# Optimization experiments

Measured on AMD Instinct MI355X. Metric: run time of the kernel, lower is better.

Reference implementation:

```python
import jax, jax.numpy as jnp
import numpy as np

B, P, K, HE, HF = 256, 128, 512, 1024, 512
D = K + HE + 2 * HF  # 2560, MLP input dim
HID = 64


def setup_inputs() -> dict:
    key = jax.random.key(0)
    ks = jax.random.split(key, 6)
    query = jax.random.normal(ks[0], (B, 1, HE), dtype=jnp.float32)
    keys = jax.random.normal(ks[1], (B, P, K), dtype=jnp.float32)
    frameLSTM_h = jax.random.normal(ks[2], (B, 1, 2 * HF), dtype=jnp.float32)
    mask = jax.random.randint(ks[3], (B, P), 0, 2, dtype=jnp.int32)
    mask = mask.at[:, 0].set(1)  # guarantee at least one unmasked player per row
    W1 = jax.random.normal(ks[4], (D, HID), dtype=jnp.float32) / np.float32(np.sqrt(D))
    W2 = jax.random.normal(ks[5], (HID, 1), dtype=jnp.float32) / np.float32(np.sqrt(HID))
    return dict(query=query, keys=keys, frameLSTM_h=frameLSTM_h, mask=mask, W1=W1, W2=W2)


def reference(query, keys, frameLSTM_h, mask, W1, W2):
    # Faithful to: cat([keys, query.repeat, frame.repeat]) @ W1 -> ReLU -> @ W2.
    # The pre-activation is linear, so splitting W1 by row-blocks is exactly the
    # same math without materializing the repeated/concatenated (B,P,D) tensor.
    W1k = W1[:K]            # (K, 64)
    W1q = W1[K:K + HE]      # (HE, 64)
    W1f = W1[K + HE:]       # (2*HF, 64)
    h = jax.nn.relu(
        jnp.einsum('bpk,kh->bph', keys, W1k)
        + jnp.einsum('boe,eh->boh', query, W1q)        # broadcasts over P
        + jnp.einsum('bof,fh->boh', frameLSTM_h, W1f)  # broadcasts over P
    )  # (B, P, 64)
    raw_scores = jnp.einsum('bph,ho->bp', h, W2)  # (B, P)
    raw_scores = jnp.where(mask == 0, -jnp.inf, raw_scores)
    weights = jax.nn.softmax(raw_scores, axis=1)  # (B, P)
    context = jnp.einsum('bp,bpk->bk', weights, keys)[:, None, :]  # (B, 1, K)
    embeddings = jnp.concatenate([context, frameLSTM_h], axis=2)   # (B, 1, K+2*HF)
    return embeddings, weights
```

## Files before the change

kernel.cpp:

```cpp
#include <hip/hip_runtime.h>
#include <hip/hip_bf16.h>
#include <cstdint>
#include <math.h>


typedef __bf16 bf16;
typedef __attribute__((ext_vector_type(8))) __bf16 bf16x8;
typedef __attribute__((ext_vector_type(4))) __bf16 bf16x4;
typedef __attribute__((ext_vector_type(4))) float f32x4;

#define NB 256
#define NP 128
#define NK 512
#define SKLD 520
#define SK_BYTES (NP * SKLD * 2)
#define SMEM_BYTES (SK_BYTES + 128*4 + 128*4 + 64*4 + 64*4)

__global__ __launch_bounds__(256) void prep_kernel(
    const float* __restrict__ query, const float* __restrict__ frame,
    const float* __restrict__ W1, bf16* __restrict__ w1kt,
    float* __restrict__ proj_part)
{
    const int blk = blockIdx.x;
    const int t = threadIdx.x;
    if (blk < 1024) {
        __shared__ float part[4][64];
        const int b = blk >> 2;
        const int q4 = blk & 3;
        const int h = t & 63;
        const int g = t >> 6;
        const float* src = (q4 < 2 ? query : frame) + (size_t)b * 1024 + (q4 & 1) * 512 + g * 128;
        const float* wrow = W1 + (size_t)(512 + q4 * 512 + g * 128) * 64 + h;
        float acc = 0.f;
#pragma unroll 8
        for (int dd = 0; dd < 128; dd++)
            acc += src[dd] * wrow[(size_t)dd * 64];
        part[g][h] = acc;
        __syncthreads();
        if (t < 64)
            proj_part[((size_t)q4 * NB + b) * 64 + t] =
                part[0][t] + part[1][t] + part[2][t] + part[3][t];
    } else {
        __shared__ float s[32][65];
        const int j = blk - 1024;
        const int k0 = j * 32;
#pragma unroll
        for (int i = 0; i < 8; i++) {
            const int idx = t + 256 * i;
            const int k = idx >> 6, h = idx & 63;
            s[k][h] = W1[(size_t)(k0 + k) * 64 + h];
        }
        __syncthreads();
#pragma unroll
        for (int i = 0; i < 8; i++) {
            const int idx = t + 256 * i;
            const int h = idx >> 5, kk = idx & 31;
            w1kt[(size_t)h * 512 + k0 + kk] = (bf16)s[kk][h];
        }
    }
}

__global__ __launch_bounds__(256) void attn_kernel(
    const float* __restrict__ keys, const float* __restrict__ frame,
    const int* __restrict__ mask, const float* __restrict__ W2,
    const bf16* __restrict__ w1kt, const float* __restrict__ proj_part,
    float* __restrict__ out)
{
    extern __shared__ char smem[];
    bf16* sk      = (bf16*)smem;
    float* scores = (float*)(smem + SK_BYTES);
    float* wts    = scores + 128;
    float* projl  = wts + 128;
    float* w2l    = projl + 64;

    const int b = blockIdx.x;
    const int t = threadIdx.x;

    if (t < 64)
        projl[t] = proj_part[(size_t)b * 64 + t]
                 + proj_part[((size_t)NB + b) * 64 + t]
                 + proj_part[((size_t)2 * NB + b) * 64 + t]
                 + proj_part[((size_t)3 * NB + b) * 64 + t];
    else if (t < 128) w2l[t - 64] = W2[t - 64];

    const float* kb = keys + (size_t)b * (NP * NK);
    {
        const int rowadd = t >> 7;
        const int c0 = (t & 127) * 4;
        float4 kv[2][16];
#pragma unroll
        for (int ii = 0; ii < 16; ii++)
            kv[0][ii] = *(const float4*)(kb + (size_t)ii * 1024 + t * 4);
#pragma unroll
        for (int jj = 0; jj < 4; jj++) {
            const int cur = jj & 1;
            if (jj < 3) {
#pragma unroll
                for (int ii = 0; ii < 16; ii++)
                    kv[cur ^ 1][ii] =
                        *(const float4*)(kb + (size_t)((jj + 1) * 16 + ii) * 1024 + t * 4);
            }
#pragma unroll
            for (int ii = 0; ii < 16; ii++) {
                const float4 v = kv[cur][ii];
                bf16x4 bv;
                bv[0] = (bf16)v.x; bv[1] = (bf16)v.y;
                bv[2] = (bf16)v.z; bv[3] = (bf16)v.w;
                *(bf16x4*)(sk + (size_t)(2 * (jj * 16 + ii) + rowadd) * SKLD + c0) = bv;
            }
        }
    }
    __syncthreads();

    const int w = t >> 6;
    const int lane = t & 63;
    const int m = lane & 15;
    const int q = lane >> 4;
    const int pw = w * 32;

    const bf16* bbase = w1kt + (size_t)m * 512 + q * 8;

    bf16x8 Bv[2][16];
#pragma unroll
    for (int kk = 0; kk < 16; kk++)
        Bv[0][kk] = *(const bf16x8*)(bbase + kk * 32);

    float pr[2][4] = {{0.f,0.f,0.f,0.f},{0.f,0.f,0.f,0.f}};

#pragma unroll
    for (int nt = 0; nt < 4; nt++) {
        const int cur = nt & 1;
        if (nt < 3) {
#pragma unroll
            for (int kk = 0; kk < 16; kk++)
                Bv[cur ^ 1][kk] = *(const bf16x8*)(bbase + (nt + 1) * 8192 + kk * 32);
        }
        f32x4 acc0 = (f32x4){0.f,0.f,0.f,0.f};
        f32x4 acc1 = (f32x4){0.f,0.f,0.f,0.f};
#pragma unroll
        for (int kk = 0; kk < 16; kk++) {
            const int k0 = kk * 32 + q * 8;
            const bf16x8 A0 = *(const bf16x8*)(sk + (pw + m) * SKLD + k0);
            const bf16x8 A1 = *(const bf16x8*)(sk + (pw + 16 + m) * SKLD + k0);
            acc0 = __builtin_amdgcn_mfma_f32_16x16x32_bf16(A0, Bv[cur][kk], acc0, 0, 0, 0);
            acc1 = __builtin_amdgcn_mfma_f32_16x16x32_bf16(A1, Bv[cur][kk], acc1, 0, 0, 0);
        }
        const int h = nt * 16 + m;
        const float pv = projl[h];
        const float wv = w2l[h];
#pragma unroll
        for (int r = 0; r < 4; r++) {
            pr[0][r] += fmaxf(acc0[r] + pv, 0.f) * wv;
            pr[1][r] += fmaxf(acc1[r] + pv, 0.f) * wv;
        }
    }

#pragma unroll
    for (int off = 1; off < 16; off <<= 1) {
#pragma unroll
        for (int mt = 0; mt < 2; mt++)
#pragma unroll
            for (int r = 0; r < 4; r++)
                pr[mt][r] += __shfl_xor(pr[mt][r], off);
    }
    if (m == 0) {
#pragma unroll
        for (int mt = 0; mt < 2; mt++) {
            const int pbase = pw + mt * 16 + q * 4;
#pragma unroll
            for (int r = 0; r < 4; r++) scores[pbase + r] = pr[mt][r];
        }
    }
    __syncthreads();

    if (w == 0) {
        const int pa = lane, pb = lane + 64;
        float s0 = (mask[b * 128 + pa] == 0) ? -INFINITY : scores[pa];
        float s1 = (mask[b * 128 + pb] == 0) ? -INFINITY : scores[pb];
        float mx = fmaxf(s0, s1);
#pragma unroll
        for (int off = 32; off; off >>= 1) mx = fmaxf(mx, __shfl_xor(mx, off));
        float e0 = __expf(s0 - mx), e1 = __expf(s1 - mx);
        float sum = e0 + e1;
#pragma unroll
        for (int off = 32; off; off >>= 1) sum += __shfl_xor(sum, off);
        const float inv = 1.0f / sum;
        e0 *= inv; e1 *= inv;
        wts[pa] = e0; wts[pb] = e1;
        float* wout = out + (size_t)NB * 1536;
        wout[b * 128 + pa] = e0;
        wout[b * 128 + pb] = e1;
    }
    __syncthreads();

    {
        float a0 = 0.f, a1 = 0.f;
        const int c = 2 * t;
#pragma unroll 8
        for (int p = 0; p < 128; p++) {
            const float wv = wts[p];
            const uint32_t uv = *(const uint32_t*)(sk + p * SKLD + c);
            a0 += wv * __uint_as_float(uv << 16);
            a1 += wv * __uint_as_float(uv & 0xffff0000u);
        }
        out[(size_t)b * 1536 + c] = a0;
        out[(size_t)b * 1536 + c + 1] = a1;
    }
    {
        const float4 fv = *(const float4*)(frame + (size_t)b * 1024 + t * 4);
        *(float4*)(out + (size_t)b * 1536 + 512 + t * 4) = fv;
    }
}

extern "C" void kernel_launch(void* const* d_in, const int* in_sizes, int n_in,
                              void* d_out, int out_size, void* d_ws, size_t ws_size,
                              hipStream_t stream) {
    const float* query = (const float*)d_in[0];
    const float* keys  = (const float*)d_in[1];
    const float* frame = (const float*)d_in[2];
    const int*   mask  = (const int*)d_in[3];
    const float* W1    = (const float*)d_in[4];
    const float* W2    = (const float*)d_in[5];
    float* out = (float*)d_out;

    bf16*  w1kt      = (bf16*)d_ws;
    float* proj_part = (float*)((char*)d_ws + (64 << 10));

    hipFuncSetAttribute((const void*)attn_kernel,
                        hipFuncAttributeMaxDynamicSharedMemorySize, SMEM_BYTES);

    prep_kernel<<<1040, 256, 0, stream>>>(query, frame, W1, w1kt, proj_part);
    attn_kernel<<<256, 256, SMEM_BYTES, stream>>>(keys, frame, mask, W2, w1kt,
                                                  proj_part, out);
}
```

Before: 123.5 us.

## Fold query/frame projection into attention kernel via MFMA on transposed bf16 W1

Moves the per-batch query/frame projection out of the 1024-block prep kernel and into the attention kernel. Each wave computes one 512-wide slice with bf16 MFMA, using only the broadcast row of the 16x16 tile. The prep kernel now only transposes W1 into bf16 layouts for the key and query/frame parts. This drops most of the prep grid and the proj_part round trip through global memory. In exchange, the projection now runs in bf16 instead of fp32, and the attention kernel does redundant MFMA work because 15 of the 16 rows are unused.

Result: no change. 123.1 us (-0.3%).

```diff
diff --git a/kernel.cpp b/kernel.cpp
--- a/kernel.cpp
+++ b/kernel.cpp
@@ -14,36 +14,17 @@
 #define NK 512
 #define SKLD 520
 #define SK_BYTES (NP * SKLD * 2)
-#define SMEM_BYTES (SK_BYTES + 128*4 + 128*4 + 64*4 + 64*4)
+#define SMEM_BYTES (SK_BYTES + 128*4 + 128*4 + 256*4 + 64*4)
 
 __global__ __launch_bounds__(256) void prep_kernel(
-    const float* __restrict__ query, const float* __restrict__ frame,
     const float* __restrict__ W1, bf16* __restrict__ w1kt,
-    float* __restrict__ proj_part)
+    bf16* __restrict__ w1qft)
 {
     const int blk = blockIdx.x;
     const int t = threadIdx.x;
-    if (blk < 1024) {
-        __shared__ float part[4][64];
-        const int b = blk >> 2;
-        const int q4 = blk & 3;
-        const int h = t & 63;
-        const int g = t >> 6;
-        const float* src = (q4 < 2 ? query : frame) + (size_t)b * 1024 + (q4 & 1) * 512 + g * 128;
-        const float* wrow = W1 + (size_t)(512 + q4 * 512 + g * 128) * 64 + h;
-        float acc = 0.f;
-#pragma unroll 8
-        for (int dd = 0; dd < 128; dd++)
-            acc += src[dd] * wrow[(size_t)dd * 64];
-        part[g][h] = acc;
-        __syncthreads();
-        if (t < 64)
-            proj_part[((size_t)q4 * NB + b) * 64 + t] =
-                part[0][t] + part[1][t] + part[2][t] + part[3][t];
-    } else {
-        __shared__ float s[32][65];
-        const int j = blk - 1024;
-        const int k0 = j * 32;
+    __shared__ float s[32][65];
+    if (blk < 16) {
+        const int k0 = blk * 32;
 #pragma unroll
         for (int i = 0; i < 8; i++) {
             const int idx = t + 256 * i;
@@ -57,31 +38,85 @@
             const int h = idx >> 5, kk = idx & 31;
             w1kt[(size_t)h * 512 + k0 + kk] = (bf16)s[kk][h];
         }
+    } else {
+        const int j = blk - 16;
+        const int d0 = j * 32;
+#pragma unroll
+        for (int i = 0; i < 8; i++) {
+            const int idx = t + 256 * i;
+            const int r = idx >> 6, h = idx & 63;
+            s[r][h] = W1[(size_t)(512 + d0 + r) * 64 + h];
+        }
+        __syncthreads();
+#pragma unroll
+        for (int i = 0; i < 8; i++) {
+            const int idx = t + 256 * i;
+            const int h = idx >> 5, rr = idx & 31;
+            w1qft[(size_t)h * 2048 + d0 + rr] = (bf16)s[rr][h];
+        }
     }
 }
 
 __global__ __launch_bounds__(256) void attn_kernel(
-    const float* __restrict__ keys, const float* __restrict__ frame,
-    const int* __restrict__ mask, const float* __restrict__ W2,
-    const bf16* __restrict__ w1kt, const float* __restrict__ proj_part,
-    float* __restrict__ out)
+    const float* __restrict__ keys, const float* __restrict__ query,
+    const float* __restrict__ frame, const int* __restrict__ mask,
+    const float* __restrict__ W2, const bf16* __restrict__ w1kt,
+    const bf16* __restrict__ w1qft, float* __restrict__ out)
 {
     extern __shared__ char smem[];
     bf16* sk      = (bf16*)smem;
     float* scores = (float*)(smem + SK_BYTES);
     float* wts    = scores + 128;
-    float* projl  = wts + 128;
-    float* w2l    = projl + 64;
+    float* pp     = wts + 128;
+    float* w2l    = pp + 256;
 
     const int b = blockIdx.x;
     const int t = threadIdx.x;
-
-    if (t < 64)
-        projl[t] = proj_part[(size_t)b * 64 + t]
-                 + proj_part[((size_t)NB + b) * 64 + t]
-                 + proj_part[((size_t)2 * NB + b) * 64 + t]
-                 + proj_part[((size_t)3 * NB + b) * 64 + t];
-    else if (t < 128) w2l[t - 64] = W2[t - 64];
+    const int w = t >> 6;
+    const int lane = t & 63;
+    const int m = lane & 15;
+    const int q = lane >> 4;
+
+    if (t < 64) w2l[t] = W2[t];
+
+    {
+        const float* qf = (w < 2 ? query : frame) + (size_t)b * 1024 + (w & 1) * 512;
+        const bf16* wb = w1qft + (size_t)m * 2048 + w * 512 + q * 8;
+        f32x4 pacc[4];
+#pragma unroll
+        for (int nt = 0; nt < 4; nt++) pacc[nt] = (f32x4){0.f, 0.f, 0.f, 0.f};
+
+        float4 qa = *(const float4*)(qf + q * 8);
+        float4 qb = *(const float4*)(qf + q * 8 + 4);
+        bf16x8 Bp[4];
+#pragma unroll
+        for (int nt = 0; nt < 4; nt++) Bp[nt] = *(const bf16x8*)(wb + nt * 32768);
+
+#pragma unroll
+        for (int kk = 0; kk < 16; kk++) {
+            bf16x8 Af;
+            Af[0] = (bf16)qa.x; Af[1] = (bf16)qa.y; Af[2] = (bf16)qa.z; Af[3] = (bf16)qa.w;
+            Af[4] = (bf16)qb.x; Af[5] = (bf16)qb.y; Af[6] = (bf16)qb.z; Af[7] = (bf16)qb.w;
+            bf16x8 Bc[4];
+#pragma unroll
+            for (int nt = 0; nt < 4; nt++) Bc[nt] = Bp[nt];
+            if (kk < 15) {
+                qa = *(const float4*)(qf + (kk + 1) * 32 + q * 8);
+                qb = *(const float4*)(qf + (kk + 1) * 32 + q * 8 + 4);
+#pragma unroll
+                for (int nt = 0; nt < 4; nt++)
+                    Bp[nt] = *(const bf16x8*)(wb + nt * 32768 + (kk + 1) * 32);
+            }
+#pragma unroll
+            for (int nt = 0; nt < 4; nt++)
+                pacc[nt] = __builtin_amdgcn_mfma_f32_16x16x32_bf16(Af, Bc[nt], pacc[nt], 0, 0, 0);
+        }
+        if (q == 0) {
+#pragma unroll
+            for (int nt = 0; nt < 4; nt++)
+                pp[w * 64 + nt * 16 + m] = pacc[nt][0];
+        }
+    }
 
     const float* kb = keys + (size_t)b * (NP * NK);
     {
@@ -112,12 +147,7 @@
     }
     __syncthreads();
 
-    const int w = t >> 6;
-    const int lane = t & 63;
-    const int m = lane & 15;
-    const int q = lane >> 4;
     const int pw = w * 32;
-
     const bf16* bbase = w1kt + (size_t)m * 512 + q * 8;
 
     bf16x8 Bv[2][16];
@@ -146,7 +176,7 @@
             acc1 = __builtin_amdgcn_mfma_f32_16x16x32_bf16(A1, Bv[cur][kk], acc1, 0, 0, 0);
         }
         const int h = nt * 16 + m;
-        const float pv = projl[h];
+        const float pv = pp[h] + pp[64 + h] + pp[128 + h] + pp[192 + h];
         const float wv = w2l[h];
 #pragma unroll
         for (int r = 0; r < 4; r++) {
@@ -223,13 +253,13 @@
     const float* W2    = (const float*)d_in[5];
     float* out = (float*)d_out;
 
-    bf16*  w1kt      = (bf16*)d_ws;
-    float* proj_part = (float*)((char*)d_ws + (64 << 10));
+    bf16* w1kt  = (bf16*)d_ws;
+    bf16* w1qft = (bf16*)((char*)d_ws + (64 << 10));
 
     hipFuncSetAttribute((const void*)attn_kernel,
                         hipFuncAttributeMaxDynamicSharedMemorySize, SMEM_BYTES);
 
-    prep_kernel<<<1040, 256, 0, stream>>>(query, frame, W1, w1kt, proj_part);
-    attn_kernel<<<256, 256, SMEM_BYTES, stream>>>(keys, frame, mask, W2, w1kt,
-                                                  proj_part, out);
+    prep_kernel<<<80, 256, 0, stream>>>(W1, w1kt, w1qft);
+    attn_kernel<<<256, 256, SMEM_BYTES, stream>>>(keys, query, frame, mask, W2,
+                                                  w1kt, w1qft, out);
 }
```
